# Performance work log

Hardware: AMD Instinct MI355X
Metric: run time of the kernel (lower is better)

## Reference

```python
import jax, jax.numpy as jnp
import numpy as np

NEG_INF = -1e9


def setup_inputs() -> dict:
    key = jax.random.key(0)
    ks = jax.random.split(key, 9)
    B, T, E, D, H = 64, 2048, 1024, 1024, 1024
    enc = jax.random.normal(ks[0], (B, T, E), dtype=jnp.float32)
    dec = jax.random.normal(ks[1], (B, D), dtype=jnp.float32)
    inp_mask = jax.random.randint(ks[2], (B, T), 0, 2, dtype=jnp.int32)
    s = 1.0 / np.sqrt(H)
    W_enc = jax.random.normal(ks[3], (E, H), dtype=jnp.float32) * s
    b_enc = jax.random.normal(ks[4], (H,), dtype=jnp.float32) * 0.01
    W_dec = jax.random.normal(ks[5], (D, H), dtype=jnp.float32) * s
    b_dec = jax.random.normal(ks[6], (H,), dtype=jnp.float32) * 0.01
    W_out = jax.random.normal(ks[7], (H, 1), dtype=jnp.float32) * s
    b_out = jax.random.normal(ks[8], (1,), dtype=jnp.float32) * 0.01
    return {"enc": enc, "dec": dec, "inp_mask": inp_mask,
            "W_enc": W_enc, "b_enc": b_enc, "W_dec": W_dec, "b_dec": b_dec,
            "W_out": W_out, "b_out": b_out}


def reference(enc, dec, inp_mask, W_enc, b_enc, W_dec, b_dec, W_out, b_out):
    # a: [B, T, H] = Linear(enc) + Linear(dec)[:, None, :]
    a = jnp.einsum('bte,eh->bth', enc, W_enc) + b_enc \
        + (dec @ W_dec + b_dec)[:, None, :]
    a = jnp.tanh(a)
    # scores: [B, T]
    scores = (jnp.einsum('bth,h->bt', a, W_out[:, 0]) + b_out[0])
    scores = jnp.where(inp_mask == 0, NEG_INF, scores)
    probs = jax.nn.softmax(scores, axis=1)            # [B, T]
    attn = jnp.einsum('bt,bte->be', probs, enc)       # [B, E]
    return (attn, probs)
```

## Files before the change

### kernel.cpp

```cpp
#include <hip/hip_runtime.h>
#include <hip/hip_bf16.h>

typedef __attribute__((ext_vector_type(4))) float f32x4;
typedef __attribute__((ext_vector_type(4))) unsigned int u32x4;
typedef __attribute__((ext_vector_type(2))) unsigned int u32x2;

static constexpr int Bb = 64;
static constexpr int Tt = 2048;
static constexpr int Ee = 1024;
static constexpr int Hh = 1024;
static constexpr int ATTN_N = Bb * Ee;
static constexpr int PROB_N = Bb * Tt;

__device__ inline unsigned short f2bf(float f) {
    __hip_bfloat16 h = __float2bfloat16(f);
    return __builtin_bit_cast(unsigned short, h);
}

__global__ void wtrans_kernel(const float* __restrict__ w_enc,
                              unsigned short* __restrict__ w16t) {
    __shared__ float tile[32][33];
    const int bx = blockIdx.x & 31;
    const int by = blockIdx.x >> 5;
    const int tx = threadIdx.x & 31;
    const int ty = threadIdx.x >> 5;
#pragma unroll
    for (int j = 0; j < 4; ++j) {
        int e = by * 32 + ty + j * 8;
        int h = bx * 32 + tx;
        tile[ty + j * 8][tx] = w_enc[e * Hh + h];
    }
    __syncthreads();
#pragma unroll
    for (int j = 0; j < 4; ++j) {
        int h = bx * 32 + ty + j * 8;
        int e = by * 32 + tx;
        w16t[h * Ee + e] = f2bf(tile[tx][ty + j * 8]);
    }
}

__global__ void ddec_kernel(const float* __restrict__ dec,
                            const float* __restrict__ w_dec,
                            const float* __restrict__ b_dec,
                            const float* __restrict__ b_enc,
                            float* __restrict__ ddec) {
    const int b = blockIdx.y;
    const int h = blockIdx.x * 256 + threadIdx.x;
    float acc = b_dec[h] + b_enc[h];
    const float* dr = dec + b * Ee;
#pragma unroll 4
    for (int e = 0; e < Ee; ++e) {
        acc += dr[e] * w_dec[e * Hh + h];
    }
    ddec[b * Hh + h] = acc;
}

__global__ __launch_bounds__(512, 2) void gemm_score_kernel(
    const float* __restrict__ enc, const unsigned short* __restrict__ w16t,
    const float* __restrict__ ddec, const float* __restrict__ w_out,
    float* __restrict__ scores) {
    __shared__ unsigned short As[128 * 64];
    __shared__ unsigned short Bs[256 * 64];

    const int tid = threadIdx.x;
    const int lane = tid & 63;
    const int wid = tid >> 6;
    const int wm = wid >> 2;
    const int wn = wid & 3;
    const int lr = lane & 15;
    const int lg = lane >> 4;

    const int g = blockIdx.x;
    const int xcd = g & 7;
    const int slot = g >> 3;
    const int ntile = slot & 3;
    const int mtile = xcd * 128 + (slot >> 2);
    const int m0 = mtile * 128;
    const int n0 = ntile * 256;
    const int bidx = m0 >> 11;

    const int arow = tid >> 4;
    const int acol = (tid & 15) * 4;
    const int brow = tid >> 3;
    const int bcol = (tid & 7) * 8;

    f32x4 areg[4];
    u32x4 breg[4];

    auto loadA = [&](int kt) {
        const float* src = enc + (size_t)m0 * Ee + kt * 64 + acol;
#pragma unroll
        for (int ci = 0; ci < 4; ++ci)
            areg[ci] = *reinterpret_cast<const f32x4*>(src + (size_t)(arow + 32 * ci) * Ee);
    };
    auto loadB = [&](int kt) {
        const unsigned short* src = w16t + (size_t)n0 * Ee + kt * 64 + bcol;
#pragma unroll
        for (int ci = 0; ci < 4; ++ci)
            breg[ci] = *reinterpret_cast<const u32x4*>(src + (size_t)(brow + 64 * ci) * Ee);
    };
    auto storeA = [&]() {
#pragma unroll
        for (int ci = 0; ci < 4; ++ci) {
            int r = arow + 32 * ci;
            int off = r * 128 + ((acol * 2) ^ ((r & 7) << 4));
            unsigned int lo = (unsigned)f2bf(areg[ci].x) | ((unsigned)f2bf(areg[ci].y) << 16);
            unsigned int hi = (unsigned)f2bf(areg[ci].z) | ((unsigned)f2bf(areg[ci].w) << 16);
            u32x2 w; w.x = lo; w.y = hi;
            *reinterpret_cast<u32x2*>((char*)As + off) = w;
        }
    };
    auto storeB = [&]() {
#pragma unroll
        for (int ci = 0; ci < 4; ++ci) {
            int r = brow + 64 * ci;
            int off = r * 128 + ((bcol * 2) ^ ((r & 7) << 4));
            *reinterpret_cast<u32x4*>((char*)Bs + off) = breg[ci];
        }
    };

    f32x4 acc[4][4];
#pragma unroll
    for (int ni = 0; ni < 4; ++ni) {
        float dv = ddec[bidx * Hh + n0 + wn * 64 + ni * 16 + lr];
#pragma unroll
        for (int mi = 0; mi < 4; ++mi) {
            acc[mi][ni].x = dv; acc[mi][ni].y = dv;
            acc[mi][ni].z = dv; acc[mi][ni].w = dv;
        }
    }

    loadA(0);
    loadB(0);

    for (int kt = 0; kt < Ee / 64; ++kt) {
        __syncthreads();
        storeA();
        storeB();
        __syncthreads();
        if (kt < Ee / 64 - 1) {
            loadA(kt + 1);
            loadB(kt + 1);
        }
#pragma unroll
        for (int kh = 0; kh < 2; ++kh) {
            const int kb = (kh * 32 + 8 * lg) * 2;
            u32x4 af[4], bf[4];
#pragma unroll
            for (int mi = 0; mi < 4; ++mi) {
                int r = wm * 64 + mi * 16 + lr;
                af[mi] = *reinterpret_cast<const u32x4*>((char*)As + r * 128 + (kb ^ ((r & 7) << 4)));
            }
#pragma unroll
            for (int ni = 0; ni < 4; ++ni) {
                int r = wn * 64 + ni * 16 + lr;
                bf[ni] = *reinterpret_cast<const u32x4*>((char*)Bs + r * 128 + (kb ^ ((r & 7) << 4)));
            }
#pragma unroll
            for (int mi = 0; mi < 4; ++mi)
#pragma unroll
                for (int ni = 0; ni < 4; ++ni)
                    asm("v_mfma_f32_16x16x32_bf16 %0, %1, %2, %0"
                        : "+v"(acc[mi][ni])
                        : "v"(af[mi]), "v"(bf[ni]));
        }
    }

    asm volatile("s_nop 7\n\ts_nop 7\n\ts_nop 7" ::: );

    float wout[4];
#pragma unroll
    for (int ni = 0; ni < 4; ++ni)
        wout[ni] = w_out[n0 + wn * 64 + ni * 16 + lr];

#pragma unroll
    for (int mi = 0; mi < 4; ++mi) {
#pragma unroll
        for (int i = 0; i < 4; ++i) {
            float s = 0.f;
#pragma unroll
            for (int ni = 0; ni < 4; ++ni) {
                float x = (i == 0) ? acc[mi][ni].x : (i == 1) ? acc[mi][ni].y
                           : (i == 2) ? acc[mi][ni].z : acc[mi][ni].w;
                float t = 1.f - 2.f / (__expf(2.f * x) + 1.f);
                s += t * wout[ni];
            }
            s += __shfl_xor(s, 1);
            s += __shfl_xor(s, 2);
            s += __shfl_xor(s, 4);
            s += __shfl_xor(s, 8);
            if (lr == 0) {
                int row = m0 + wm * 64 + mi * 16 + 4 * lg + i;
                atomicAdd(&scores[row], s);
            }
        }
    }
}

__global__ __launch_bounds__(256) void softmax_kernel(float* __restrict__ sc,
                                                      const int* __restrict__ mask) {
    __shared__ float red[256];
    const int b = blockIdx.x;
    const int tid = threadIdx.x;
    float* row = sc + b * Tt;
    const int* mrow = mask + b * Tt;

    float v[8];
    float mx = -3.0e38f;
#pragma unroll
    for (int j = 0; j < 8; ++j) {
        int t = tid + j * 256;
        float s = row[t];
        v[j] = (mrow[t] == 0) ? -1.0e9f : s;
        mx = fmaxf(mx, v[j]);
    }
    red[tid] = mx;
    __syncthreads();
    for (int off = 128; off > 0; off >>= 1) {
        if (tid < off) red[tid] = fmaxf(red[tid], red[tid + off]);
        __syncthreads();
    }
    mx = red[0];
    __syncthreads();

    float p[8];
    float sum = 0.f;
#pragma unroll
    for (int j = 0; j < 8; ++j) {
        p[j] = __expf(v[j] - mx);
        sum += p[j];
    }
    red[tid] = sum;
    __syncthreads();
    for (int off = 128; off > 0; off >>= 1) {
        if (tid < off) red[tid] += red[tid + off];
        __syncthreads();
    }
    float inv = 1.f / red[0];
#pragma unroll
    for (int j = 0; j < 8; ++j)
        row[tid + j * 256] = p[j] * inv;
}

__global__ __launch_bounds__(256) void attn_kernel(const float* __restrict__ enc,
                                                   const float* __restrict__ probs,
                                                   float* __restrict__ attn) {
    __shared__ float pr[128];
    const int b = blockIdx.y;
    const int tc = blockIdx.x;
    const int tid = threadIdx.x;
    if (tid < 128) pr[tid] = probs[b * Tt + tc * 128 + tid];
    __syncthreads();

    const int e0 = tid * 4;
    f32x4 acc; acc.x = 0.f; acc.y = 0.f; acc.z = 0.f; acc.w = 0.f;
    const float* base = enc + (size_t)b * Tt * Ee + (size_t)tc * 128 * Ee + e0;
#pragma unroll 4
    for (int t = 0; t < 128; ++t) {
        f32x4 vv = *reinterpret_cast<const f32x4*>(base + (size_t)t * Ee);
        float pw = pr[t];
        acc.x += pw * vv.x; acc.y += pw * vv.y;
        acc.z += pw * vv.z; acc.w += pw * vv.w;
    }
    atomicAdd(&attn[b * Ee + e0 + 0], acc.x);
    atomicAdd(&attn[b * Ee + e0 + 1], acc.y);
    atomicAdd(&attn[b * Ee + e0 + 2], acc.z);
    atomicAdd(&attn[b * Ee + e0 + 3], acc.w);
}

extern "C" void kernel_launch(void* const* d_in, const int* in_sizes, int n_in,
                              void* d_out, int out_size, void* d_ws, size_t ws_size,
                              hipStream_t stream) {
    const float* enc      = (const float*)d_in[0];
    const float* dec      = (const float*)d_in[1];
    const int*   inp_mask = (const int*)d_in[2];
    const float* W_enc    = (const float*)d_in[3];
    const float* b_enc    = (const float*)d_in[4];
    const float* W_dec    = (const float*)d_in[5];
    const float* b_dec    = (const float*)d_in[6];
    const float* W_out    = (const float*)d_in[7];

    float* attn   = (float*)d_out;
    float* scores = (float*)d_out + ATTN_N;

    unsigned short* w16t = (unsigned short*)d_ws;
    float* ddec = attn;

    hipMemsetAsync(scores, 0, (size_t)PROB_N * sizeof(float), stream);

    wtrans_kernel<<<dim3(1024), 256, 0, stream>>>(W_enc, w16t);
    ddec_kernel<<<dim3(4, 64), 256, 0, stream>>>(dec, W_dec, b_dec, b_enc, ddec);
    gemm_score_kernel<<<dim3(4096), 512, 0, stream>>>(enc, w16t, ddec, W_out, scores);

    hipMemsetAsync(attn, 0, (size_t)ATTN_N * sizeof(float), stream);

    softmax_kernel<<<dim3(64), 256, 0, stream>>>(scores, inp_mask);
    attn_kernel<<<dim3(16, 64), 256, 0, stream>>>(enc, scores, attn);
}
```

Measured before the change: 675.3 us.

## Double-buffer LDS tiles in GEMM-score kernel with single barrier per k-step

Splits the shared-memory A and B tiles into two buffers so the next k-tile is converted and stored while MFMAs consume the current one. Global loads are issued two tiles ahead, and each iteration uses one barrier instead of two. Wave priority is raised around the MFMA block. The doubled LDS footprint may reduce the number of resident blocks per CU.

```diff
diff --git a/kernel.cpp b/kernel.cpp
--- a/kernel.cpp
+++ b/kernel.cpp
@@ -59,8 +59,8 @@
     const float* __restrict__ enc, const unsigned short* __restrict__ w16t,
     const float* __restrict__ ddec, const float* __restrict__ w_out,
     float* __restrict__ scores) {
-    __shared__ unsigned short As[128 * 64];
-    __shared__ unsigned short Bs[256 * 64];
+    __shared__ unsigned short As[2][128 * 64];
+    __shared__ unsigned short Bs[2][256 * 64];
 
     const int tid = threadIdx.x;
     const int lane = tid & 63;
@@ -99,7 +99,8 @@
         for (int ci = 0; ci < 4; ++ci)
             breg[ci] = *reinterpret_cast<const u32x4*>(src + (size_t)(brow + 64 * ci) * Ee);
     };
-    auto storeA = [&]() {
+    auto storeA = [&](int db) {
+        char* base = (char*)&As[db][0];
 #pragma unroll
         for (int ci = 0; ci < 4; ++ci) {
             int r = arow + 32 * ci;
@@ -107,15 +108,16 @@
             unsigned int lo = (unsigned)f2bf(areg[ci].x) | ((unsigned)f2bf(areg[ci].y) << 16);
             unsigned int hi = (unsigned)f2bf(areg[ci].z) | ((unsigned)f2bf(areg[ci].w) << 16);
             u32x2 w; w.x = lo; w.y = hi;
-            *reinterpret_cast<u32x2*>((char*)As + off) = w;
-        }
-    };
-    auto storeB = [&]() {
+            *reinterpret_cast<u32x2*>(base + off) = w;
+        }
+    };
+    auto storeB = [&](int db) {
+        char* base = (char*)&Bs[db][0];
 #pragma unroll
         for (int ci = 0; ci < 4; ++ci) {
             int r = brow + 64 * ci;
             int off = r * 128 + ((bcol * 2) ^ ((r & 7) << 4));
-            *reinterpret_cast<u32x4*>((char*)Bs + off) = breg[ci];
+            *reinterpret_cast<u32x4*>(base + off) = breg[ci];
         }
     };
 
@@ -130,40 +132,58 @@
         }
     }
 
+    auto mfma_half = [&](int db, int kh) {
+        const int kb = (kh * 32 + 8 * lg) * 2;
+        const char* abase = (const char*)&As[db][0];
+        const char* bbase = (const char*)&Bs[db][0];
+        u32x4 af[4], bf[4];
+#pragma unroll
+        for (int mi = 0; mi < 4; ++mi) {
+            int r = wm * 64 + mi * 16 + lr;
+            af[mi] = *reinterpret_cast<const u32x4*>(abase + r * 128 + (kb ^ ((r & 7) << 4)));
+        }
+#pragma unroll
+        for (int ni = 0; ni < 4; ++ni) {
+            int r = wn * 64 + ni * 16 + lr;
+            bf[ni] = *reinterpret_cast<const u32x4*>(bbase + r * 128 + (kb ^ ((r & 7) << 4)));
+        }
+        __builtin_amdgcn_s_setprio(1);
+#pragma unroll
+        for (int mi = 0; mi < 4; ++mi)
+#pragma unroll
+            for (int ni = 0; ni < 4; ++ni)
+                asm("v_mfma_f32_16x16x32_bf16 %0, %1, %2, %0"
+                    : "+v"(acc[mi][ni])
+                    : "v"(af[mi]), "v"(bf[ni]));
+        __builtin_amdgcn_s_setprio(0);
+    };
+
     loadA(0);
     loadB(0);
-
+    storeA(0);
+    storeB(0);
+    loadA(1);
+    loadB(1);
+    asm volatile("s_waitcnt lgkmcnt(0)" ::: "memory");
+    __builtin_amdgcn_s_barrier();
+    asm volatile("" ::: "memory");
+
+    int db = 0;
     for (int kt = 0; kt < Ee / 64; ++kt) {
-        __syncthreads();
-        storeA();
-        storeB();
-        __syncthreads();
+        mfma_half(db, 0);
         if (kt < Ee / 64 - 1) {
-            loadA(kt + 1);
-            loadB(kt + 1);
-        }
-#pragma unroll
-        for (int kh = 0; kh < 2; ++kh) {
-            const int kb = (kh * 32 + 8 * lg) * 2;
-            u32x4 af[4], bf[4];
-#pragma unroll
-            for (int mi = 0; mi < 4; ++mi) {
-                int r = wm * 64 + mi * 16 + lr;
-                af[mi] = *reinterpret_cast<const u32x4*>((char*)As + r * 128 + (kb ^ ((r & 7) << 4)));
-            }
-#pragma unroll
-            for (int ni = 0; ni < 4; ++ni) {
-                int r = wn * 64 + ni * 16 + lr;
-                bf[ni] = *reinterpret_cast<const u32x4*>((char*)Bs + r * 128 + (kb ^ ((r & 7) << 4)));
-            }
-#pragma unroll
-            for (int mi = 0; mi < 4; ++mi)
-#pragma unroll
-                for (int ni = 0; ni < 4; ++ni)
-                    asm("v_mfma_f32_16x16x32_bf16 %0, %1, %2, %0"
-                        : "+v"(acc[mi][ni])
-                        : "v"(af[mi]), "v"(bf[ni]));
-        }
+            storeA(db ^ 1);
+            storeB(db ^ 1);
+        }
+        if (kt < Ee / 64 - 2) {
+            loadA(kt + 2);
+            loadB(kt + 2);
+        }
+        mfma_half(db, 1);
+        asm volatile("s_waitcnt lgkmcnt(0)" ::: "memory");
+        __builtin_amdgcn_s_barrier();
+        asm volatile("" ::: "memory");
+        db ^= 1;
     }
 
     asm volatile("s_nop 7\n\ts_nop 7\n\ts_nop 7" ::: );
```

Result: faster. 645.7 us (-4.4%).

## Double-buffer GEMM LDS with direct global-to-LDS B loads and 256-row tiles

Applied to the files above, without the earlier changes.

Restructures the fused enc@W_enc GEMM to use 256x256 output tiles instead of 128x256, which halves the grid and doubles per-wave accumulators. The W tile now goes straight from global memory into a double-buffered LDS region via global_load_lds. The A tile (fp32 enc converted to bf16) is prefetched into registers and written into the alternate buffer while MFMAs run on the current one, using explicit barriers, waitcnts and setprio. The aim is to overlap memory traffic with MFMA work and to reduce re-reads of W and enc. The trade-off is 64KB of LDS per block and 128 accumulator VGPRs, which may lower occupancy below the 2 blocks requested in launch_bounds.

```diff
diff --git a/kernel.cpp b/kernel.cpp
--- a/kernel.cpp
+++ b/kernel.cpp
@@ -3,7 +3,6 @@
 
 typedef __attribute__((ext_vector_type(4))) float f32x4;
 typedef __attribute__((ext_vector_type(4))) unsigned int u32x4;
-typedef __attribute__((ext_vector_type(2))) unsigned int u32x2;
 
 static constexpr int Bb = 64;
 static constexpr int Tt = 2048;
@@ -15,6 +14,13 @@
 __device__ inline unsigned short f2bf(float f) {
     __hip_bfloat16 h = __float2bfloat16(f);
     return __builtin_bit_cast(unsigned short, h);
+}
+
+__device__ inline void gload_lds16(const unsigned short* g, unsigned short* l) {
+    __builtin_amdgcn_global_load_lds(
+        (const __attribute__((address_space(1))) void*)g,
+        (__attribute__((address_space(3))) void*)l,
+        16, 0, 0);
 }
 
 __global__ void wtrans_kernel(const float* __restrict__ w_enc,
@@ -59,8 +65,8 @@
     const float* __restrict__ enc, const unsigned short* __restrict__ w16t,
     const float* __restrict__ ddec, const float* __restrict__ w_out,
     float* __restrict__ scores) {
-    __shared__ unsigned short As[128 * 64];
-    __shared__ unsigned short Bs[256 * 64];
+    __shared__ unsigned short As[2][256 * 64];
+    __shared__ unsigned short Bs[2][256 * 64];
 
     const int tid = threadIdx.x;
     const int lane = tid & 63;
@@ -74,96 +80,126 @@
     const int xcd = g & 7;
     const int slot = g >> 3;
     const int ntile = slot & 3;
-    const int mtile = xcd * 128 + (slot >> 2);
-    const int m0 = mtile * 128;
+    const int mtile = xcd * 64 + (slot >> 2);
+    const int m0 = mtile * 256;
     const int n0 = ntile * 256;
     const int bidx = m0 >> 11;
 
-    const int arow = tid >> 4;
-    const int acol = (tid & 15) * 4;
-    const int brow = tid >> 3;
-    const int bcol = (tid & 7) * 8;
-
-    f32x4 areg[4];
-    u32x4 breg[4];
+    const int ar = tid >> 3;
+    const int as = tid & 7;
+
+    f32x4 aregs[8];
 
     auto loadA = [&](int kt) {
-        const float* src = enc + (size_t)m0 * Ee + kt * 64 + acol;
-#pragma unroll
-        for (int ci = 0; ci < 4; ++ci)
-            areg[ci] = *reinterpret_cast<const f32x4*>(src + (size_t)(arow + 32 * ci) * Ee);
-    };
-    auto loadB = [&](int kt) {
-        const unsigned short* src = w16t + (size_t)n0 * Ee + kt * 64 + bcol;
-#pragma unroll
-        for (int ci = 0; ci < 4; ++ci)
-            breg[ci] = *reinterpret_cast<const u32x4*>(src + (size_t)(brow + 64 * ci) * Ee);
-    };
-    auto storeA = [&]() {
+        const float* src = enc + (size_t)(m0 + ar) * Ee + kt * 64 + as * 8;
 #pragma unroll
         for (int ci = 0; ci < 4; ++ci) {
-            int r = arow + 32 * ci;
-            int off = r * 128 + ((acol * 2) ^ ((r & 7) << 4));
-            unsigned int lo = (unsigned)f2bf(areg[ci].x) | ((unsigned)f2bf(areg[ci].y) << 16);
-            unsigned int hi = (unsigned)f2bf(areg[ci].z) | ((unsigned)f2bf(areg[ci].w) << 16);
-            u32x2 w; w.x = lo; w.y = hi;
-            *reinterpret_cast<u32x2*>((char*)As + off) = w;
-        }
-    };
-    auto storeB = [&]() {
+            aregs[ci * 2]     = *reinterpret_cast<const f32x4*>(src + (size_t)(64 * ci) * Ee);
+            aregs[ci * 2 + 1] = *reinterpret_cast<const f32x4*>(src + (size_t)(64 * ci) * Ee + 4);
+        }
+    };
+    auto writeA = [&](int db) {
+        char* abase = (char*)&As[db][0];
 #pragma unroll
         for (int ci = 0; ci < 4; ++ci) {
-            int r = brow + 64 * ci;
-            int off = r * 128 + ((bcol * 2) ^ ((r & 7) << 4));
-            *reinterpret_cast<u32x4*>((char*)Bs + off) = breg[ci];
-        }
-    };
-
-    f32x4 acc[4][4];
+            int r = ar + 64 * ci;
+            u32x4 w;
+            w.x = (unsigned)f2bf(aregs[2 * ci].x) | ((unsigned)f2bf(aregs[2 * ci].y) << 16);
+            w.y = (unsigned)f2bf(aregs[2 * ci].z) | ((unsigned)f2bf(aregs[2 * ci].w) << 16);
+            w.z = (unsigned)f2bf(aregs[2 * ci + 1].x) | ((unsigned)f2bf(aregs[2 * ci + 1].y) << 16);
+            w.w = (unsigned)f2bf(aregs[2 * ci + 1].z) | ((unsigned)f2bf(aregs[2 * ci + 1].w) << 16);
+            *reinterpret_cast<u32x4*>(abase + r * 128 + ((as * 16) ^ ((r & 7) << 4))) = w;
+        }
+    };
+    auto stageB = [&](int kt, int db) {
+        const int sg = (lane & 7) ^ (lane >> 3);
+#pragma unroll
+        for (int c = 0; c < 4; ++c) {
+            int rr = (wid * 4 + c) * 8 + (lane >> 3);
+            const unsigned short* src = w16t + (size_t)(n0 + rr) * Ee + kt * 64 + sg * 8;
+            gload_lds16(src, &Bs[db][(wid * 4 + c) * 512]);
+        }
+    };
+
+    f32x4 acc[8][4];
 #pragma unroll
     for (int ni = 0; ni < 4; ++ni) {
         float dv = ddec[bidx * Hh + n0 + wn * 64 + ni * 16 + lr];
 #pragma unroll
-        for (int mi = 0; mi < 4; ++mi) {
+        for (int mi = 0; mi < 8; ++mi) {
             acc[mi][ni].x = dv; acc[mi][ni].y = dv;
             acc[mi][ni].z = dv; acc[mi][ni].w = dv;
         }
     }
 
+    u32x4 af[4], bf[4];
+    auto readB4 = [&](int db, int kh) {
+        const char* bbase = (const char*)&Bs[db][0];
+        const int kb = kh * 64 + lg * 16;
+#pragma unroll
+        for (int ni = 0; ni < 4; ++ni) {
+            int r = wn * 64 + ni * 16 + lr;
+            bf[ni] = *reinterpret_cast<const u32x4*>(bbase + r * 128 + (kb ^ ((r & 7) << 4)));
+        }
+    };
+    auto readA4 = [&](int db, int kh, int mib) {
+        const char* abase = (const char*)&As[db][0];
+        const int kb = kh * 64 + lg * 16;
+#pragma unroll
+        for (int k = 0; k < 4; ++k) {
+            int r = wm * 128 + (mib + k) * 16 + lr;
+            af[k] = *reinterpret_cast<const u32x4*>(abase + r * 128 + (kb ^ ((r & 7) << 4)));
+        }
+    };
+    auto mfma16 = [&](int mib) {
+        __builtin_amdgcn_s_setprio(1);
+#pragma unroll
+        for (int k = 0; k < 4; ++k)
+#pragma unroll
+            for (int ni = 0; ni < 4; ++ni)
+                asm("v_mfma_f32_16x16x32_bf16 %0, %1, %2, %0"
+                    : "+v"(acc[mib + k][ni])
+                    : "v"(af[k]), "v"(bf[ni]));
+        __builtin_amdgcn_s_setprio(0);
+    };
+
+#define BARRIER() do { asm volatile("" ::: "memory"); \
+    __builtin_amdgcn_s_barrier(); asm volatile("" ::: "memory"); } while (0)
+#define LGKM0() asm volatile("s_waitcnt lgkmcnt(0)" ::: "memory")
+#define VM0()   asm volatile("s_waitcnt vmcnt(0)" ::: "memory")
+
     loadA(0);
-    loadB(0);
-
-    for (int kt = 0; kt < Ee / 64; ++kt) {
-        __syncthreads();
-        storeA();
-        storeB();
-        __syncthreads();
-        if (kt < Ee / 64 - 1) {
-            loadA(kt + 1);
-            loadB(kt + 1);
-        }
-#pragma unroll
-        for (int kh = 0; kh < 2; ++kh) {
-            const int kb = (kh * 32 + 8 * lg) * 2;
-            u32x4 af[4], bf[4];
-#pragma unroll
-            for (int mi = 0; mi < 4; ++mi) {
-                int r = wm * 64 + mi * 16 + lr;
-                af[mi] = *reinterpret_cast<const u32x4*>((char*)As + r * 128 + (kb ^ ((r & 7) << 4)));
-            }
-#pragma unroll
-            for (int ni = 0; ni < 4; ++ni) {
-                int r = wn * 64 + ni * 16 + lr;
-                bf[ni] = *reinterpret_cast<const u32x4*>((char*)Bs + r * 128 + (kb ^ ((r & 7) << 4)));
-            }
-#pragma unroll
-            for (int mi = 0; mi < 4; ++mi)
-#pragma unroll
-                for (int ni = 0; ni < 4; ++ni)
-                    asm("v_mfma_f32_16x16x32_bf16 %0, %1, %2, %0"
-                        : "+v"(acc[mi][ni])
-                        : "v"(af[mi]), "v"(bf[ni]));
-        }
+    stageB(0, 0);
+    writeA(0);
+    LGKM0();
+    VM0();
+    BARRIER();
+
+#pragma unroll 1
+    for (int t = 0; t < 16; ++t) {
+        const int cur = t & 1;
+        const bool stage = (t < 15);
+        readB4(cur, 0);
+        readA4(cur, 0, 0);
+        if (stage) { stageB(t + 1, cur ^ 1); loadA(t + 1); }
+        BARRIER(); LGKM0();
+        mfma16(0);
+        BARRIER();
+        readA4(cur, 0, 4);
+        BARRIER(); LGKM0();
+        mfma16(4);
+        BARRIER();
+        readB4(cur, 1);
+        readA4(cur, 1, 0);
+        if (stage) writeA(cur ^ 1);
+        BARRIER(); LGKM0();
+        mfma16(0);
+        BARRIER();
+        readA4(cur, 1, 4);
+        if (stage) VM0();
+        BARRIER(); LGKM0();
+        mfma16(4);
+        BARRIER();
     }
 
     asm volatile("s_nop 7\n\ts_nop 7\n\ts_nop 7" ::: );
@@ -174,7 +210,7 @@
         wout[ni] = w_out[n0 + wn * 64 + ni * 16 + lr];
 
 #pragma unroll
-    for (int mi = 0; mi < 4; ++mi) {
+    for (int mi = 0; mi < 8; ++mi) {
 #pragma unroll
         for (int i = 0; i < 4; ++i) {
             float s = 0.f;
@@ -190,11 +226,14 @@
             s += __shfl_xor(s, 4);
             s += __shfl_xor(s, 8);
             if (lr == 0) {
-                int row = m0 + wm * 64 + mi * 16 + 4 * lg + i;
+                int row = m0 + wm * 128 + mi * 16 + 4 * lg + i;
                 atomicAdd(&scores[row], s);
             }
         }
     }
+#undef BARRIER
+#undef LGKM0
+#undef VM0
 }
 
 __global__ __launch_bounds__(256) void softmax_kernel(float* __restrict__ sc,
@@ -290,7 +329,7 @@
 
     wtrans_kernel<<<dim3(1024), 256, 0, stream>>>(W_enc, w16t);
     ddec_kernel<<<dim3(4, 64), 256, 0, stream>>>(dec, W_dec, b_dec, b_enc, ddec);
-    gemm_score_kernel<<<dim3(4096), 512, 0, stream>>>(enc, w16t, ddec, W_out, scores);
+    gemm_score_kernel<<<dim3(2048), 512, 0, stream>>>(enc, w16t, ddec, W_out, scores);
 
     hipMemsetAsync(attn, 0, (size_t)ATTN_N * sizeof(float), stream);
 
```

Measured after the change: 665.4 us. Within noise of the previous version (-1.5%).
